# Kernel optimization log

Measured on AMD Instinct MI355X. Metric: run time of the kernel, lower is better.

The kernel has to match this reference:

```python
import jax, jax.numpy as jnp
import numpy as np

NUM_HEADS = 16
NEG_FILL = -10000.0  # matches torch masked_fill value in source


def setup_inputs() -> dict:
    key = jax.random.key(0)
    ks = jax.random.split(key, 8)
    B, S, H = 4, 2048, 1024
    sc = 1.0 / np.sqrt(H)
    x = jax.random.normal(ks[0], (B, S, H), dtype=jnp.float32)
    L = jax.random.randint(ks[1], (B,), 1, S + 1, dtype=jnp.int64 if jax.config.jax_enable_x64 else jnp.int32)
    Wq = jax.random.normal(ks[2], (H, H), dtype=jnp.float32) * sc
    Wk = jax.random.normal(ks[3], (H, H), dtype=jnp.float32) * sc
    Wv = jax.random.normal(ks[4], (H, H), dtype=jnp.float32) * sc
    bv = jax.random.normal(ks[5], (H,), dtype=jnp.float32) * 0.01
    Wo = jax.random.normal(ks[6], (H, H), dtype=jnp.float32) * sc
    bo = jax.random.normal(ks[7], (H,), dtype=jnp.float32) * 0.01
    return {"x": x, "L": L, "Wq": Wq, "Wk": Wk, "Wv": Wv, "bv": bv, "Wo": Wo, "bo": bo}


def reference(x, L, Wq, Wk, Wv, bv, Wo, bo):
    # AttentionAggregator.forward with L given; dropout in eval mode (identity).
    B, S, H = x.shape
    nh = NUM_HEADS
    dk = H // nh
    # torch nn.Linear: y = x @ W.T + b
    q = (x @ Wq.T).reshape(B, S, nh, dk).transpose(0, 2, 1, 3)  # (B,h,S,dk)
    k = (x @ Wk.T).reshape(B, S, nh, dk).transpose(0, 2, 1, 3)
    v = (x @ Wv.T + bv).reshape(B, S, nh, dk).transpose(0, 2, 1, 3)
    scores = jnp.einsum("bhqd,bhkd->bhqk", q, k) / jnp.sqrt(jnp.float32(dk))
    valid = jnp.arange(S)[None, :] < L[:, None]  # (B,S) True where real token
    scores = jnp.where(valid[:, None, None, :], scores, NEG_FILL)
    attn = jax.nn.softmax(scores, axis=-1)
    ctx = jnp.einsum("bhqk,bhkd->bhqd", attn, v)
    ctx = ctx.transpose(0, 2, 1, 3).reshape(B, S, H)
    attn_out = ctx @ Wo.T + bo  # (B,S,H)
    # masked mean pool over valid positions
    m = valid.astype(x.dtype)  # (B,S)
    pooled = jnp.einsum("bsh,bs->bh", attn_out, m) / m.sum(axis=1, keepdims=True)
    return pooled
```

## Files before the change

kernel.cpp:

```cpp
#include <hip/hip_runtime.h>
#include <hip/hip_bf16.h>
#include <math.h>

constexpr int Bc = 4, Sc = 2048, Hc = 1024, NHc = 16, DKc = 64;

constexpr size_t XHOFF = 0;
constexpr size_t QOFF  = 4194304;
constexpr size_t KOFF  = 8388608;
constexpr size_t WQOFF = 12582912;
constexpr size_t WKOFF = 13107200;
constexpr size_t LIOFF = 13631488;
constexpr size_t WOFF  = 13762560;
constexpr size_t YOFF  = 13893632;
constexpr size_t CSOFF = 13959168;
constexpr size_t YPOFF = 13963264;

typedef __attribute__((ext_vector_type(8))) short bf16x8;
typedef __attribute__((ext_vector_type(4))) float f32x4;

__device__ inline short f2bf(float v) {
    __hip_bfloat16 h = __float2bfloat16(v);
    return *reinterpret_cast<short*>(&h);
}

__device__ inline float ex2(float x) {
#if defined(__has_builtin) && __has_builtin(__builtin_amdgcn_exp2f)
    return __builtin_amdgcn_exp2f(x);
#else
    float r; asm("v_exp_f32 %0, %1" : "=v"(r) : "v"(x)); return r;
#endif
}

__device__ inline void gld_lds16(const void* g, void* l) {
    __builtin_amdgcn_global_load_lds(
        (const __attribute__((address_space(1))) unsigned int*)g,
        (__attribute__((address_space(3))) unsigned int*)l, 16, 0, 0);
}

__global__ __launch_bounds__(256) void cvt_all_kernel(
    const float* __restrict__ x, const float* __restrict__ Wq,
    const float* __restrict__ Wk, float* __restrict__ ws)
{
    const size_t i = ((size_t)blockIdx.x * 256 + threadIdx.x) * 8;
    const float* src; short* dst; float scale; size_t off;
    constexpr float QSC = 0.125f * 1.44269504088896340736f;
    if (i < 8388608)       { src = x;  dst = (short*)(ws + XHOFF); off = i;            scale = 1.0f; }
    else if (i < 9437184)  { src = Wq; dst = (short*)(ws + WQOFF); off = i - 8388608;  scale = QSC;  }
    else                   { src = Wk; dst = (short*)(ws + WKOFF); off = i - 9437184;  scale = 1.0f; }
    float4 a = *(const float4*)(src + off);
    float4 b = *(const float4*)(src + off + 4);
    bf16x8 o;
    o[0] = f2bf(a.x * scale); o[1] = f2bf(a.y * scale);
    o[2] = f2bf(a.z * scale); o[3] = f2bf(a.w * scale);
    o[4] = f2bf(b.x * scale); o[5] = f2bf(b.y * scale);
    o[6] = f2bf(b.z * scale); o[7] = f2bf(b.w * scale);
    *(bf16x8*)(dst + off) = o;
}

__global__ __launch_bounds__(256) void proj_mfma_kernel(
    const int* __restrict__ L, float* __restrict__ ws)
{
    const int z  = blockIdx.z;
    const int m0 = blockIdx.y * 128;
    const int n0 = blockIdx.x * 128;
    const int b  = m0 >> 11;
    const int s0 = m0 & 2047;
    const int Lb = L[b];
    if (s0 >= Lb) return;

    const short* __restrict__ A = (const short*)(ws + XHOFF);
    const short* __restrict__ W = (const short*)(ws + (z == 0 ? WQOFF : WKOFF));
    short* __restrict__ Out = (short*)(ws + (z == 0 ? QOFF : KOFF));

    __shared__ __align__(16) short As[128 * 32];
    __shared__ __align__(16) short Bs[128 * 32];

    const int tid  = threadIdx.x;
    const int lane = tid & 63;
    const int wave = tid >> 6;
    const int l16  = lane & 15, quad = lane >> 4;
    const int wm = (wave & 1) * 64, wn = (wave >> 1) * 64;

    const int c0 = tid, c1 = tid + 256;
    const int r0 = c0 >> 2, g0 = (c0 & 3) * 8;
    const int r1 = c1 >> 2, g1 = (c1 & 3) * 8;
    short* lA0 = As + wave * 512;
    short* lA1 = As + 2048 + wave * 512;
    short* lB0 = Bs + wave * 512;
    short* lB1 = Bs + 2048 + wave * 512;

    const f32x4 z4 = {0.f, 0.f, 0.f, 0.f};
    f32x4 acc[4][4];
    #pragma unroll
    for (int i = 0; i < 4; ++i)
        #pragma unroll
        for (int j = 0; j < 4; ++j) acc[i][j] = z4;

    for (int k0 = 0; k0 < Hc; k0 += 32) {
        __syncthreads();
        gld_lds16(A + (size_t)(m0 + r0) * Hc + k0 + g0, lA0);
        gld_lds16(A + (size_t)(m0 + r1) * Hc + k0 + g1, lA1);
        gld_lds16(W + (size_t)(n0 + r0) * Hc + k0 + g0, lB0);
        gld_lds16(W + (size_t)(n0 + r1) * Hc + k0 + g1, lB1);
        __syncthreads();

        bf16x8 af[4], bfr[4];
        #pragma unroll
        for (int mt = 0; mt < 4; ++mt)
            af[mt] = *(const bf16x8*)(As + (wm + mt * 16 + l16) * 32 + quad * 8);
        #pragma unroll
        for (int nt = 0; nt < 4; ++nt)
            bfr[nt] = *(const bf16x8*)(Bs + (wn + nt * 16 + l16) * 32 + quad * 8);
        #pragma unroll
        for (int mt = 0; mt < 4; ++mt)
            #pragma unroll
            for (int nt = 0; nt < 4; ++nt)
                acc[mt][nt] = __builtin_amdgcn_mfma_f32_16x16x32_bf16(
                    af[mt], bfr[nt], acc[mt][nt], 0, 0, 0);
    }

    #pragma unroll
    for (int mt = 0; mt < 4; ++mt) {
        #pragma unroll
        for (int nt = 0; nt < 4; ++nt) {
            const int n = n0 + wn + nt * 16 + l16;
            const int h = n >> 6, d = n & 63;
            #pragma unroll
            for (int r = 0; r < 4; ++r) {
                const int s = s0 + wm + mt * 16 + quad * 4 + r;
                Out[(((size_t)b * NHc + h) * Sc + s) * DKc + d] =
                    f2bf(acc[mt][nt][r]);
            }
        }
    }
}

__global__ __launch_bounds__(256) void rowsum_kernel(
    const int* __restrict__ L, float* __restrict__ ws)
{
    const int bh = blockIdx.x;
    const int qs = blockIdx.y;
    const int b  = bh >> 4;
    const int Lb = L[b];
    if (qs * 256 >= Lb) return;

    const int tid  = threadIdx.x;
    const int wave = tid >> 6;
    const int lane = tid & 63;
    const int l16 = lane & 15, quad = lane >> 4;
    const int q0 = qs * 256 + wave * 64;

    const short* __restrict__ qarr = (const short*)(ws + QOFF) + (size_t)bh * Sc * DKc;
    const short* __restrict__ karr = (const short*)(ws + KOFF) + (size_t)bh * Sc * DKc;

    __shared__ __align__(16) short Ks[256 * 64];

    bf16x8 bq[4][2];
    #pragma unroll
    for (int g = 0; g < 4; ++g) {
        const short* qr = qarr + (size_t)(q0 + g * 16 + l16) * DKc;
        bq[g][0] = *(const bf16x8*)(qr + quad * 8);
        bq[g][1] = *(const bf16x8*)(qr + 32 + quad * 8);
    }
    float lacc[4] = {0.f, 0.f, 0.f, 0.f};

    const int nst = (Lb + 255) >> 8;
    for (int st = 0; st < nst; ++st) {
        const int kt = st << 8;
        if (st) __syncthreads();
        #pragma unroll
        for (int i = 0; i < 8; ++i) {
            const int s = i * 256 + tid;
            const int row = s >> 3, c = (s & 7) ^ (row & 7);
            gld_lds16(karr + (size_t)(kt + row) * DKc + c * 8,
                      Ks + (i * 256 + wave * 64) * 8);
        }
        __syncthreads();

        const int kmax = Lb - kt;
        if (kmax >= 256) {
            #pragma unroll
            for (int tt = 0; tt < 16; ++tt) {
                const int r = tt * 16 + l16;
                const bf16x8 alo = *(const bf16x8*)(Ks + (r * 8 + (quad ^ (r & 7))) * 8);
                const bf16x8 ahi = *(const bf16x8*)(Ks + (r * 8 + ((4 + quad) ^ (r & 7))) * 8);
                #pragma unroll
                for (int g = 0; g < 4; ++g) {
                    f32x4 c = {0.f, 0.f, 0.f, 0.f};
                    c = __builtin_amdgcn_mfma_f32_16x16x32_bf16(alo, bq[g][0], c, 0, 0, 0);
                    c = __builtin_amdgcn_mfma_f32_16x16x32_bf16(ahi, bq[g][1], c, 0, 0, 0);
                    lacc[g] += (ex2(c[0]) + ex2(c[1])) + (ex2(c[2]) + ex2(c[3]));
                }
            }
        } else {
            const int nstp = (kmax + 15) >> 4;
            for (int tt = 0; tt < nstp; ++tt) {
                const int r = tt * 16 + l16;
                const bf16x8 alo = *(const bf16x8*)(Ks + (r * 8 + (quad ^ (r & 7))) * 8);
                const bf16x8 ahi = *(const bf16x8*)(Ks + (r * 8 + ((4 + quad) ^ (r & 7))) * 8);
                #pragma unroll
                for (int g = 0; g < 4; ++g) {
                    f32x4 c = {0.f, 0.f, 0.f, 0.f};
                    c = __builtin_amdgcn_mfma_f32_16x16x32_bf16(alo, bq[g][0], c, 0, 0, 0);
                    c = __builtin_amdgcn_mfma_f32_16x16x32_bf16(ahi, bq[g][1], c, 0, 0, 0);
                    #pragma unroll
                    for (int rr = 0; rr < 4; ++rr) {
                        const bool kv = (kt + tt * 16 + quad * 4 + rr) < Lb;
                        lacc[g] += kv ? ex2(c[rr]) : 0.f;
                    }
                }
            }
        }
    }
    #pragma unroll
    for (int g = 0; g < 4; ++g) {
        lacc[g] += __shfl_xor(lacc[g], 16, 64);
        lacc[g] += __shfl_xor(lacc[g], 32, 64);
    }
    float* __restrict__ li = ws + LIOFF + (size_t)bh * Sc;
    #pragma unroll
    for (int g = 0; g < 4; ++g)
        if (quad == g) li[q0 + g * 16 + l16] = 1.0f / lacc[g];
}

__global__ __launch_bounds__(256) void colsum_kernel(
    const int* __restrict__ L, float* __restrict__ ws)
{
    const int bh = blockIdx.x;
    const int ks = blockIdx.y;
    const int b  = bh >> 4;
    const int Lb = L[b];
    if (ks * 256 >= Lb) return;

    const int tid  = threadIdx.x;
    const int wave = tid >> 6;
    const int lane = tid & 63;
    const int l16 = lane & 15, quad = lane >> 4;
    const int k0 = ks * 256 + wave * 64;

    const short* __restrict__ qarr = (const short*)(ws + QOFF) + (size_t)bh * Sc * DKc;
    const short* __restrict__ karr = (const short*)(ws + KOFF) + (size_t)bh * Sc * DKc;
    const float* __restrict__ liarr = ws + LIOFF + (size_t)bh * Sc;

    __shared__ __align__(16) short Qs[256 * 64];
    __shared__ __align__(16) float Lis[256];

    bf16x8 ak[4][2];
    #pragma unroll
    for (int g = 0; g < 4; ++g) {
        const short* kr = karr + (size_t)(k0 + g * 16 + l16) * DKc;
        ak[g][0] = *(const bf16x8*)(kr + quad * 8);
        ak[g][1] = *(const bf16x8*)(kr + 32 + quad * 8);
    }
    f32x4 w[4];
    #pragma unroll
    for (int g = 0; g < 4; ++g) w[g] = (f32x4){0.f, 0.f, 0.f, 0.f};

    const int nst = (Lb + 255) >> 8;
    for (int st = 0; st < nst; ++st) {
        const int qt = st << 8;
        if (st) __syncthreads();
        #pragma unroll
        for (int i = 0; i < 8; ++i) {
            const int s = i * 256 + tid;
            const int row = s >> 3, c = (s & 7) ^ (row & 7);
            gld_lds16(qarr + (size_t)(qt + row) * DKc + c * 8,
                      Qs + (i * 256 + wave * 64) * 8);
        }
        if (tid < 64)
            gld_lds16(liarr + qt + tid * 4, Lis);
        __syncthreads();

        const int qmax = Lb - qt;
        const int nstp = (qmax >= 256) ? 16 : ((qmax + 15) >> 4);
        for (int tt = 0; tt < nstp; ++tt) {
            const int r = tt * 16 + l16;
            const bf16x8 blo = *(const bf16x8*)(Qs + (r * 8 + (quad ^ (r & 7))) * 8);
            const bf16x8 bhi = *(const bf16x8*)(Qs + (r * 8 + ((4 + quad) ^ (r & 7))) * 8);
            const float lv = (qt + r < Lb) ? Lis[r] : 0.f;
            #pragma unroll
            for (int g = 0; g < 4; ++g) {
                f32x4 c = {0.f, 0.f, 0.f, 0.f};
                c = __builtin_amdgcn_mfma_f32_16x16x32_bf16(ak[g][0], blo, c, 0, 0, 0);
                c = __builtin_amdgcn_mfma_f32_16x16x32_bf16(ak[g][1], bhi, c, 0, 0, 0);
                #pragma unroll
                for (int rr = 0; rr < 4; ++rr)
                    w[g][rr] += ex2(c[rr]) * lv;
            }
        }
    }
    #pragma unroll
    for (int off = 1; off <= 8; off <<= 1)
        #pragma unroll
        for (int g = 0; g < 4; ++g)
            #pragma unroll
            for (int rr = 0; rr < 4; ++rr)
                w[g][rr] += __shfl_xor(w[g][rr], off, 64);
    if (l16 == 0) {
        float* __restrict__ warr = ws + WOFF + (size_t)bh * Sc;
        #pragma unroll
        for (int g = 0; g < 4; ++g)
            #pragma unroll
            for (int rr = 0; rr < 4; ++rr)
                warr[k0 + g * 16 + quad * 4 + rr] = w[g][rr];
    }
}

__global__ __launch_bounds__(256) void yw_part_kernel(
    const float* __restrict__ x, const int* __restrict__ L,
    float* __restrict__ ws)
{
    const int b  = blockIdx.y;
    const int j0 = blockIdx.x * 64;
    const int s0 = blockIdx.z * 128;
    const int Lb = L[b];
    if (s0 >= Lb) return;
    const int js = threadIdx.x & 63;
    const int sl = threadIdx.x >> 6;
    const float* __restrict__ warr = ws + WOFF + (size_t)b * NHc * Sc;
    const float* __restrict__ xb = x + (size_t)b * Sc * Hc;

    __shared__ float wt[128][20];
    __shared__ float red[4][16][64];

    #pragma unroll
    for (int i = 0; i < 8; ++i) {
        const int s = (threadIdx.x & 15) + 16 * i;
        const int h = threadIdx.x >> 4;
        float v = 0.f;
        if (s0 + s < Lb) v = warr[(size_t)h * Sc + s0 + s];
        wt[s][h] = v;
    }
    __syncthreads();

    float acc[16];
    #pragma unroll
    for (int h = 0; h < 16; ++h) acc[h] = 0.f;

    #pragma unroll 4
    for (int s = sl; s < 128; s += 4) {
        const float xv = xb[(size_t)(s0 + s) * Hc + j0 + js];
        const f32x4 wa = *(const f32x4*)&wt[s][0];
        const f32x4 wb = *(const f32x4*)&wt[s][4];
        const f32x4 wc = *(const f32x4*)&wt[s][8];
        const f32x4 wd = *(const f32x4*)&wt[s][12];
        #pragma unroll
        for (int h = 0; h < 4; ++h) acc[h]      += wa[h] * xv;
        #pragma unroll
        for (int h = 0; h < 4; ++h) acc[4 + h]  += wb[h] * xv;
        #pragma unroll
        for (int h = 0; h < 4; ++h) acc[8 + h]  += wc[h] * xv;
        #pragma unroll
        for (int h = 0; h < 4; ++h) acc[12 + h] += wd[h] * xv;
    }
    #pragma unroll
    for (int h = 0; h < 16; ++h) red[sl][h][js] = acc[h];
    __syncthreads();
    if (sl == 0) {
        float* __restrict__ yp = ws + YPOFF +
            ((size_t)blockIdx.z * Bc * NHc + (size_t)b * NHc) * Hc;
        #pragma unroll
        for (int h = 0; h < 16; ++h)
            yp[(size_t)h * Hc + j0 + js] =
                red[0][h][js] + red[1][h][js] + red[2][h][js] + red[3][h][js];
    }
}

__global__ __launch_bounds__(256) void yw_reduce_kernel(
    const int* __restrict__ L, float* __restrict__ ws)
{
    const int b = blockIdx.y;
    const int i = blockIdx.x * 256 + threadIdx.x;
    const int nc = (L[b] + 127) >> 7;
    const float* __restrict__ p = ws + YPOFF + (size_t)b * NHc * Hc + i;
    float acc = 0.f;
    for (int c = 0; c < nc; ++c)
        acc += p[(size_t)c * Bc * NHc * Hc];
    ws[YOFF + (size_t)b * NHc * Hc + i] = acc;
}

__global__ __launch_bounds__(256) void csum_kernel(
    const float* __restrict__ Wv, const float* __restrict__ bv,
    const int* __restrict__ L, float* __restrict__ ws)
{
    const int b = blockIdx.y;
    const int h = blockIdx.x;
    const int n0 = h * 64;
    const int lane = threadIdx.x & 63;
    const int wave = threadIdx.x >> 6;
    const float Lb = (float)L[b];

    __shared__ float ys[1024];
    const float* __restrict__ y = ws + YOFF + ((size_t)b * NHc + h) * Hc;
    for (int i = threadIdx.x; i < 1024; i += 256) ys[i] = y[i];
    __syncthreads();

    f32x4 yv[4];
    #pragma unroll
    for (int p = 0; p < 4; ++p) yv[p] = *(const f32x4*)&ys[p * 256 + lane * 4];

    #pragma unroll
    for (int r = 0; r < 16; ++r) {
        const int n = n0 + wave * 16 + r;
        const float* wrow = Wv + (size_t)n * Hc;
        float a = 0.f;
        #pragma unroll
        for (int p = 0; p < 4; ++p) {
            const f32x4 wv = *(const f32x4*)(wrow + p * 256 + lane * 4);
            a += wv[0]*yv[p][0] + wv[1]*yv[p][1] + wv[2]*yv[p][2] + wv[3]*yv[p][3];
        }
        #pragma unroll
        for (int off = 32; off > 0; off >>= 1) a += __shfl_xor(a, off, 64);
        if (lane == 0)
            ws[CSOFF + (size_t)b * Hc + n] = a + bv[n] * Lb;
    }
}

__global__ __launch_bounds__(256) void out_kernel(
    const float* __restrict__ Wo, const float* __restrict__ bo,
    const int* __restrict__ L, const float* __restrict__ ws,
    float* __restrict__ out)
{
    const int b = blockIdx.y;
    const int o0 = blockIdx.x * 64;
    const int lane = threadIdx.x & 63;
    const int wave = threadIdx.x >> 6;
    const float linv = 1.0f / (float)L[b];

    __shared__ float cs[1024];
    const float* __restrict__ c = ws + CSOFF + (size_t)b * Hc;
    for (int i = threadIdx.x; i < 1024; i += 256) cs[i] = c[i];
    __syncthreads();

    f32x4 cv[4];
    #pragma unroll
    for (int p = 0; p < 4; ++p) cv[p] = *(const f32x4*)&cs[p * 256 + lane * 4];

    #pragma unroll
    for (int r = 0; r < 16; ++r) {
        const int o = o0 + wave * 16 + r;
        const float* wrow = Wo + (size_t)o * Hc;
        float a = 0.f;
        #pragma unroll
        for (int p = 0; p < 4; ++p) {
            const f32x4 wv = *(const f32x4*)(wrow + p * 256 + lane * 4);
            a += wv[0]*cv[p][0] + wv[1]*cv[p][1] + wv[2]*cv[p][2] + wv[3]*cv[p][3];
        }
        #pragma unroll
        for (int off = 32; off > 0; off >>= 1) a += __shfl_xor(a, off, 64);
        if (lane == 0)
            out[(size_t)b * Hc + o] = a * linv + bo[o];
    }
}

extern "C" void kernel_launch(void* const* d_in, const int* in_sizes, int n_in,
                              void* d_out, int out_size, void* d_ws, size_t ws_size,
                              hipStream_t stream)
{
    (void)in_sizes; (void)n_in; (void)out_size; (void)ws_size;
    const float* x  = (const float*)d_in[0];
    const int*   L  = (const int*)d_in[1];
    const float* Wq = (const float*)d_in[2];
    const float* Wk = (const float*)d_in[3];
    const float* Wv = (const float*)d_in[4];
    const float* bv = (const float*)d_in[5];
    const float* Wo = (const float*)d_in[6];
    const float* bo = (const float*)d_in[7];
    float* out = (float*)d_out;
    float* ws  = (float*)d_ws;

    cvt_all_kernel<<<5120, 256, 0, stream>>>(x, Wq, Wk, ws);

    dim3 gp(Hc / 128, (Bc * Sc) / 128, 2);
    proj_mfma_kernel<<<gp, 256, 0, stream>>>(L, ws);

    dim3 gr(Bc * NHc, Sc / 256);
    rowsum_kernel<<<gr, 256, 0, stream>>>(L, ws);
    colsum_kernel<<<gr, 256, 0, stream>>>(L, ws);

    dim3 gy(Hc / 64, Bc, Sc / 128);
    yw_part_kernel<<<gy, 256, 0, stream>>>(x, L, ws);

    dim3 gyr((NHc * Hc) / 256, Bc);
    yw_reduce_kernel<<<gyr, 256, 0, stream>>>(L, ws);

    dim3 gc(NHc, Bc);
    csum_kernel<<<gc, 256, 0, stream>>>(Wv, bv, L, ws);

    dim3 go(Hc / 64, Bc);
    out_kernel<<<go, 256, 0, stream>>>(Wo, bo, L, ws, out);
}
```

Measured before the change: 249.6 us.

## Pipeline K/Q tile loads per wave with triple-buffered LDS and vmcnt waits

The rowsum and colsum kernels now stream K (or Q) in 32-row chunks that each wave loads into its own 3-slot LDS ring. Waits use s_waitcnt vmcnt instead of block-wide __syncthreads, so loads overlap with MFMA compute. In colsum the full row-inverse array is loaded into LDS once up front rather than per tile. Each wave now fetches the same K/Q data redundantly, which raises global/L2 traffic. LDS use grows to about 48KB plus 8KB, which may reduce occupancy.

```diff
diff --git a/kernel.cpp b/kernel.cpp
--- a/kernel.cpp
+++ b/kernel.cpp
@@ -153,7 +153,11 @@
     const short* __restrict__ qarr = (const short*)(ws + QOFF) + (size_t)bh * Sc * DKc;
     const short* __restrict__ karr = (const short*)(ws + KOFF) + (size_t)bh * Sc * DKc;
 
-    __shared__ __align__(16) short Ks[256 * 64];
+    __shared__ __align__(16) short Ks[4][3][32 * 64];
+
+    const int srow = lane >> 3;
+    const int scol = (lane & 7) ^ srow;
+    const short* ksrc = karr + (size_t)srow * DKc + scol * 8;
 
     bf16x8 bq[4][2];
     #pragma unroll
@@ -164,26 +168,33 @@
     }
     float lacc[4] = {0.f, 0.f, 0.f, 0.f};
 
-    const int nst = (Lb + 255) >> 8;
-    for (int st = 0; st < nst; ++st) {
-        const int kt = st << 8;
-        if (st) __syncthreads();
-        #pragma unroll
-        for (int i = 0; i < 8; ++i) {
-            const int s = i * 256 + tid;
-            const int row = s >> 3, c = (s & 7) ^ (row & 7);
-            gld_lds16(karr + (size_t)(kt + row) * DKc + c * 8,
-                      Ks + (i * 256 + wave * 64) * 8);
-        }
-        __syncthreads();
-
-        const int kmax = Lb - kt;
-        if (kmax >= 256) {
-            #pragma unroll
-            for (int tt = 0; tt < 16; ++tt) {
+    const int n = (Lb + 31) >> 5;
+
+    auto stage = [&](int s, int kt) {
+        short* dst = &Ks[wave][s][0];
+        #pragma unroll
+        for (int j = 0; j < 4; ++j)
+            gld_lds16(ksrc + (size_t)(kt + j * 8) * DKc, dst + j * 512);
+    };
+
+    stage(0, 0);
+    if (n > 1) stage(1, 32);
+    if (n > 2) stage(2, 64);
+
+    int slot = 0;
+    for (int t = 0; t < n; ++t) {
+        const int kt = t << 5;
+        if (t + 2 < n)      asm volatile("s_waitcnt vmcnt(8)" ::: "memory");
+        else if (t + 1 < n) asm volatile("s_waitcnt vmcnt(4)" ::: "memory");
+        else                asm volatile("s_waitcnt vmcnt(0)" ::: "memory");
+
+        const short* B = &Ks[wave][slot][0];
+        if (kt + 32 <= Lb) {
+            #pragma unroll
+            for (int tt = 0; tt < 2; ++tt) {
                 const int r = tt * 16 + l16;
-                const bf16x8 alo = *(const bf16x8*)(Ks + (r * 8 + (quad ^ (r & 7))) * 8);
-                const bf16x8 ahi = *(const bf16x8*)(Ks + (r * 8 + ((4 + quad) ^ (r & 7))) * 8);
+                const bf16x8 alo = *(const bf16x8*)(B + r * 64 + (quad ^ (r & 7)) * 8);
+                const bf16x8 ahi = *(const bf16x8*)(B + r * 64 + ((4 + quad) ^ (r & 7)) * 8);
                 #pragma unroll
                 for (int g = 0; g < 4; ++g) {
                     f32x4 c = {0.f, 0.f, 0.f, 0.f};
@@ -193,11 +204,11 @@
                 }
             }
         } else {
-            const int nstp = (kmax + 15) >> 4;
-            for (int tt = 0; tt < nstp; ++tt) {
+            #pragma unroll
+            for (int tt = 0; tt < 2; ++tt) {
                 const int r = tt * 16 + l16;
-                const bf16x8 alo = *(const bf16x8*)(Ks + (r * 8 + (quad ^ (r & 7))) * 8);
-                const bf16x8 ahi = *(const bf16x8*)(Ks + (r * 8 + ((4 + quad) ^ (r & 7))) * 8);
+                const bf16x8 alo = *(const bf16x8*)(B + r * 64 + (quad ^ (r & 7)) * 8);
+                const bf16x8 ahi = *(const bf16x8*)(B + r * 64 + ((4 + quad) ^ (r & 7)) * 8);
                 #pragma unroll
                 for (int g = 0; g < 4; ++g) {
                     f32x4 c = {0.f, 0.f, 0.f, 0.f};
@@ -211,7 +222,10 @@
                 }
             }
         }
-    }
+        if (t + 3 < n) stage(slot, kt + 96);
+        slot = (slot == 2) ? 0 : slot + 1;
+    }
+
     #pragma unroll
     for (int g = 0; g < 4; ++g) {
         lacc[g] += __shfl_xor(lacc[g], 16, 64);
@@ -242,8 +256,8 @@
     const short* __restrict__ karr = (const short*)(ws + KOFF) + (size_t)bh * Sc * DKc;
     const float* __restrict__ liarr = ws + LIOFF + (size_t)bh * Sc;
 
-    __shared__ __align__(16) short Qs[256 * 64];
-    __shared__ __align__(16) float Lis[256];
+    __shared__ __align__(16) short Qs[4][3][32 * 64];
+    __shared__ __align__(16) float Lis[2048];
 
     bf16x8 ak[4][2];
     #pragma unroll
@@ -252,32 +266,49 @@
         ak[g][0] = *(const bf16x8*)(kr + quad * 8);
         ak[g][1] = *(const bf16x8*)(kr + 32 + quad * 8);
     }
+
+    #pragma unroll
+    for (int j2 = 0; j2 < 2; ++j2)
+        gld_lds16(liarr + wave * 512 + j2 * 256 + lane * 4,
+                  &Lis[wave * 512 + j2 * 256]);
+    __syncthreads();
+
+    const int srow = lane >> 3;
+    const int scol = (lane & 7) ^ srow;
+    const short* qsrc = qarr + (size_t)srow * DKc + scol * 8;
+
     f32x4 w[4];
     #pragma unroll
     for (int g = 0; g < 4; ++g) w[g] = (f32x4){0.f, 0.f, 0.f, 0.f};
 
-    const int nst = (Lb + 255) >> 8;
-    for (int st = 0; st < nst; ++st) {
-        const int qt = st << 8;
-        if (st) __syncthreads();
-        #pragma unroll
-        for (int i = 0; i < 8; ++i) {
-            const int s = i * 256 + tid;
-            const int row = s >> 3, c = (s & 7) ^ (row & 7);
-            gld_lds16(qarr + (size_t)(qt + row) * DKc + c * 8,
-                      Qs + (i * 256 + wave * 64) * 8);
-        }
-        if (tid < 64)
-            gld_lds16(liarr + qt + tid * 4, Lis);
-        __syncthreads();
-
-        const int qmax = Lb - qt;
-        const int nstp = (qmax >= 256) ? 16 : ((qmax + 15) >> 4);
-        for (int tt = 0; tt < nstp; ++tt) {
+    const int n = (Lb + 31) >> 5;
+
+    auto stage = [&](int s, int qt) {
+        short* dst = &Qs[wave][s][0];
+        #pragma unroll
+        for (int j = 0; j < 4; ++j)
+            gld_lds16(qsrc + (size_t)(qt + j * 8) * DKc, dst + j * 512);
+    };
+
+    stage(0, 0);
+    if (n > 1) stage(1, 32);
+    if (n > 2) stage(2, 64);
+
+    int slot = 0;
+    for (int t = 0; t < n; ++t) {
+        const int qt = t << 5;
+        if (t + 2 < n)      asm volatile("s_waitcnt vmcnt(8)" ::: "memory");
+        else if (t + 1 < n) asm volatile("s_waitcnt vmcnt(4)" ::: "memory");
+        else                asm volatile("s_waitcnt vmcnt(0)" ::: "memory");
+
+        const short* B = &Qs[wave][slot][0];
+        const bool full = (qt + 32 <= Lb);
+        #pragma unroll
+        for (int tt = 0; tt < 2; ++tt) {
             const int r = tt * 16 + l16;
-            const bf16x8 blo = *(const bf16x8*)(Qs + (r * 8 + (quad ^ (r & 7))) * 8);
-            const bf16x8 bhi = *(const bf16x8*)(Qs + (r * 8 + ((4 + quad) ^ (r & 7))) * 8);
-            const float lv = (qt + r < Lb) ? Lis[r] : 0.f;
+            const bf16x8 blo = *(const bf16x8*)(B + r * 64 + (quad ^ (r & 7)) * 8);
+            const bf16x8 bhi = *(const bf16x8*)(B + r * 64 + ((4 + quad) ^ (r & 7)) * 8);
+            const float lv = (full || qt + r < Lb) ? Lis[qt + r] : 0.f;
             #pragma unroll
             for (int g = 0; g < 4; ++g) {
                 f32x4 c = {0.f, 0.f, 0.f, 0.f};
@@ -288,7 +319,10 @@
                     w[g][rr] += ex2(c[rr]) * lv;
             }
         }
-    }
+        if (t + 3 < n) stage(slot, qt + 96);
+        slot = (slot == 2) ? 0 : slot + 1;
+    }
+
     #pragma unroll
     for (int off = 1; off <= 8; off <<= 1)
         #pragma unroll
```

Result: slower. 261.8 us (+4.9%).
